# Optimization experiments

Hardware: AMD Instinct MI355X
Metric: run time of the kernel (lower is better)

The kernel has to match this reference:

```python
import math
import jax, jax.numpy as jnp
import numpy as np

DIM = 3
NB = 8  # 2**DIM blades, grade-sorted: [1, e1, e2, e3, e12, e13, e23, e123]
GRADE_SLICES = [(0, 1), (1, 4), (4, 7), (7, 8)]
SUBSPACES = [1, 3, 3, 1]
GRADE_IDX = np.repeat(np.arange(4), SUBSPACES)  # blade -> grade index
EPS = 1e-6
SQRT2 = math.sqrt(2.0)


def _build_cayley():
    # Cl(3,0) Euclidean Cayley table, blades sorted by (grade, bitmask).
    masks = sorted(range(NB), key=lambda m: (bin(m).count("1"), m))
    pos = {m: i for i, m in enumerate(masks)}
    cay = np.zeros((NB, NB, NB), dtype=np.float32)
    for i, mi in enumerate(masks):
        for k, mk in enumerate(masks):
            a, s = mi >> 1, 0
            while a:
                s += bin(a & mk).count("1")
                a >>= 1
            cay[i, pos[mi ^ mk], k] = -1.0 if (s & 1) else 1.0
    triples = []
    for gi in range(4):
        for gj in range(4):
            for gk in range(4):
                (i0, i1), (j0, j1), (k0, k1) = GRADE_SLICES[gi], GRADE_SLICES[gj], GRADE_SLICES[gk]
                if np.any(cay[i0:i1, j0:j1, k0:k1] != 0):
                    triples.append((gi, gj, gk))
    return cay, triples

CAYLEY_NP, TRIPLES = _build_cayley()
NPATHS = len(TRIPLES)  # 20 nonzero grade-triple paths for Cl(3,0)


def mv_linear(x, w, b=None):
    # x: [B,n,8]; w: [m,n,4] (one weight per grade subspace); bias -> scalar blade only.
    w8 = w[..., GRADE_IDX]  # [m,n,8]
    out = jnp.einsum("bni,mni->bmi", x, w8)
    if b is not None:
        out = out.at[..., 0].add(b)
    return out


def grade_q(x):
    # per-grade squared magnitude (Euclidean metric -> all blade signs +1): [B,n,8]->[B,n,4]
    return jnp.stack([jnp.sum(x[..., s:e] ** 2, axis=-1) for s, e in GRADE_SLICES], axis=-1)


def normalization(x, a):
    # CGENN NormalizationLayer (init=0): interpolate per-grade norm toward 1 via sigmoid gate.
    norms = jnp.sqrt(grade_q(x))  # [B,n,4]
    sa = jax.nn.sigmoid(a)  # [n,4]
    norms = sa[None] * (norms - 1.0) + 1.0
    return x / (norms[..., GRADE_IDX] + EPS)


def mv_silu(x, a, b):
    # MVSiLU with invariant='mag2': gate on [scalar, q_grade1, q_grade2, q_grade3].
    q = grade_q(x)  # [B,n,4]
    inv = jnp.concatenate([x[..., :1], q[..., 1:]], axis=-1)  # [B,n,4]
    gate = a[None] * inv + b[None]
    return jax.nn.sigmoid(gate[..., GRADE_IDX]) * x


def fc_geometric_product(x, xr, w, cayley):
    # out[b,m,j] = sum_{n,i,k} x[b,n,i] * cayley[i,j,k] * W[m,n,path(gi,gj,gk)] * xr[b,n,k]
    B, n = x.shape[0], x.shape[1]
    m = w.shape[0]
    out = jnp.zeros((B, m, NB), dtype=x.dtype)
    for t, (gi, gj, gk) in enumerate(TRIPLES):
        (i0, i1), (j0, j1), (k0, k1) = GRADE_SLICES[gi], GRADE_SLICES[gj], GRADE_SLICES[gk]
        tmp = jnp.einsum("bni,ijk,bnk->bnj", x[..., i0:i1], cayley[i0:i1, j0:j1, k0:k1], xr[..., k0:k1])
        out = out.at[:, :, j0:j1].add(jnp.einsum("bnj,mn->bmj", tmp, w[:, :, t]))
    return out


def cw_geometric_product(x, xr, w, cayley):
    # channel-wise steerable GP: out[b,n,j] = sum_{i,k} x[b,n,i]*cayley[i,j,k]*w[n,path]*xr[b,n,k]
    out = jnp.zeros_like(x)
    for t, (gi, gj, gk) in enumerate(TRIPLES):
        (i0, i1), (j0, j1), (k0, k1) = GRADE_SLICES[gi], GRADE_SLICES[gj], GRADE_SLICES[gk]
        tmp = jnp.einsum("bni,ijk,bnk->bnj", x[..., i0:i1], cayley[i0:i1, j0:j1, k0:k1], xr[..., k0:k1])
        out = out.at[:, :, j0:j1].add(tmp * w[None, :, t, None])
    return out


B, IN, HID, OUT = 1024, 256, 512, 128


def setup_inputs():
    key = jax.random.key(0)
    ks = jax.random.split(key, 16)

    def nrm(k, shape, std):
        return jax.random.normal(k, shape, dtype=jnp.float32) * std

    s_in = 1.0 / math.sqrt(IN)
    s_hid = 1.0 / math.sqrt(HID)
    return {
        "x": jax.random.normal(ks[0], (B, IN, NB), dtype=jnp.float32),
        "lr1_w": nrm(ks[1], (IN, IN, 4), s_in),
        "n1_a": jnp.zeros((IN, 4), jnp.float32),
        "ll1_w": nrm(ks[2], (HID, IN, 4), s_in),
        "ll1_b": jnp.zeros((HID,), jnp.float32),
        "w1": nrm(ks[3], (HID, IN, NPATHS), 1.0 / math.sqrt(IN * (DIM + 1))),
        "act_a": jnp.ones((HID, 4), jnp.float32),
        "act_b": jnp.zeros((HID, 4), jnp.float32),
        "lrg_w": nrm(ks[4], (HID, HID, 4), s_hid),
        "ng_a": jnp.zeros((HID, 4), jnp.float32),
        "llg_w": nrm(ks[5], (HID, HID, 4), s_hid),
        "llg_b": jnp.zeros((HID,), jnp.float32),
        "wg": nrm(ks[6], (HID, NPATHS), 1.0 / math.sqrt(DIM + 1)),
        "lr2_w": nrm(ks[7], (HID, HID, 4), s_hid),
        "n2_a": jnp.zeros((HID, 4), jnp.float32),
        "ll2_w": nrm(ks[8], (OUT, HID, 4), s_hid),
        "ll2_b": jnp.zeros((OUT,), jnp.float32),
        "w2": nrm(ks[9], (OUT, HID, NPATHS), 1.0 / math.sqrt(HID * (DIM + 1))),
    }


def reference(x, lr1_w, n1_a, ll1_w, ll1_b, w1, act_a, act_b,
              lrg_w, ng_a, llg_w, llg_b, wg,
              lr2_w, n2_a, ll2_w, ll2_b, w2):
    cayley = jnp.asarray(CAYLEY_NP)
    # fcgp1: right linear -> normalize -> weighted geometric product + first-order term
    xr = normalization(mv_linear(x, lr1_w), n1_a)
    h = (mv_linear(x, ll1_w, ll1_b) + fc_geometric_product(x, xr, w1, cayley)) / SQRT2
    h = mv_silu(h, act_a, act_b)
    # channel-wise steerable geometric product layer
    hr = normalization(mv_linear(h, lrg_w), ng_a)
    h = (mv_linear(h, llg_w, llg_b) + cw_geometric_product(h, hr, wg, cayley)) / SQRT2
    h = mv_silu(h, act_a, act_b)
    # fcgp2
    hr = normalization(mv_linear(h, lr2_w), n2_a)
    out = (mv_linear(h, ll2_w, ll2_b) + fc_geometric_product(h, hr, w2, cayley)) / SQRT2
    return out
```

## Files before the change

### kernel.cpp

```cpp
#include <hip/hip_runtime.h>
#include <math.h>


typedef unsigned short u16;
typedef __attribute__((ext_vector_type(8))) short short8;
typedef __attribute__((ext_vector_type(4))) float f32x4;

#define RSQRT2F 0.70710678118654752440f

__device__ constexpr int PP_I[64] = {
  0,0,0,0,0,0,0,0,  1,1,1,1,1,1,1,1,  2,2,2,2,2,2,2,2,  3,3,3,3,3,3,3,3,
  4,4,4,4,4,4,4,4,  5,5,5,5,5,5,5,5,  6,6,6,6,6,6,6,6,  7,7,7,7,7,7,7,7};
__device__ constexpr int PP_K[64] = {
  0,1,2,3,4,5,6,7,  0,1,2,3,4,5,6,7,  0,1,2,3,4,5,6,7,  0,1,2,3,4,5,6,7,
  0,1,2,3,4,5,6,7,  0,1,2,3,4,5,6,7,  0,1,2,3,4,5,6,7,  0,1,2,3,4,5,6,7};
__device__ constexpr int PP_C[64] = {
   0, 1, 2, 3, 4, 5, 6, 7,
   9, 8,15,16,13,14,21,20,
  10,15, 8,17,12,21,14,19,
  11,16,17, 8,21,12,13,18,
  29,24,23,35,22,34,33,28,
  30,25,35,23,34,22,32,27,
  31,35,25,24,33,32,22,26,
  43,42,41,40,39,38,37,36};
__device__ constexpr int PP_T[64] = {
   0, 1, 1, 1, 2, 2, 2, 3,
   5, 4, 7, 7, 6, 6, 9, 8,
   5, 7, 4, 7, 6, 9, 6, 8,
   5, 7, 7, 4, 9, 6, 6, 8,
  13,11,11,15,10,14,14,12,
  13,11,15,11,14,10,14,12,
  13,15,11,11,14,14,10,12,
  19,18,18,18,17,17,17,16};
__device__ constexpr int PP_J[64] = {
  0,1,2,3,4,5,6,7,
  1,0,4,5,2,3,7,6,
  2,4,0,6,1,7,3,5,
  3,5,6,0,7,1,2,4,
  4,2,1,7,0,6,5,3,
  5,3,7,1,6,0,4,2,
  6,7,3,2,5,4,0,1,
  7,6,5,4,3,2,1,0};
__device__ constexpr float PP_S[64] = {
  1, 1, 1, 1, 1, 1, 1, 1,
  1, 1, 1, 1, 1, 1, 1, 1,
  1,-1, 1, 1,-1,-1, 1,-1,
  1,-1,-1, 1, 1,-1,-1, 1,
  1,-1, 1, 1,-1,-1, 1,-1,
  1,-1,-1, 1, 1,-1,-1, 1,
  1, 1,-1, 1,-1, 1,-1,-1,
  1, 1,-1, 1,-1, 1,-1,-1};

__device__ constexpr int GJ_CNT[8] = {4,6,6,6,6,6,6,4};
__device__ constexpr int GJ_C[8][6] = {
  {0,8,22,36,0,0},
  {1,9,12,23,26,37},
  {2,10,13,24,27,38},
  {3,11,14,25,28,39},
  {4,15,18,29,32,40},
  {5,16,19,30,33,41},
  {6,17,20,31,34,42},
  {7,21,35,43,0,0}};
__device__ constexpr int GJ_T[8][6] = {
  {0,4,10,16,0,0},
  {1,5,6,11,12,17},
  {1,5,6,11,12,17},
  {1,5,6,11,12,17},
  {2,7,8,13,14,18},
  {2,7,8,13,14,18},
  {2,7,8,13,14,18},
  {3,9,15,19,0,0}};
__device__ constexpr int GRADE[8] = {0,1,1,1,2,2,2,3};

__device__ inline float sigm(float x) { return 1.0f / (1.0f + expf(-x)); }
__device__ inline u16 f2bf(float f) {
  unsigned u = __float_as_uint(f);
  return (u16)((u + 0x7fffu + ((u >> 16) & 1u)) >> 16);
}
__device__ inline float bf2f(u16 h) { return __uint_as_float(((unsigned)h) << 16); }

#define BT 128
#define MT 128
#define BKc 64

__global__ __launch_bounds__(256) void mfma_gemm(
    const u16* __restrict__ Alin, const u16* __restrict__ Pfeat,
    const u16* __restrict__ WLin, const u16* __restrict__ WLin2,
    const u16* __restrict__ WGp,
    float* __restrict__ out1, float* __restrict__ out2,
    int N, int M, int aug, int planeA, int planeO, int KSbits, int KCbits)
{
  const int zz    = blockIdx.z;
  const int set   = zz >> (3 + KSbits);
  const int rem   = zz & ((8 << KSbits) - 1);
  const int j     = rem >> KSbits;
  const int slice = rem & ((1 << KSbits) - 1);
  const u16* WL   = set ? WLin2 : WLin;
  float* outp     = set ? out2 : out1;

  const int b0   = blockIdx.y * BT;
  const int m0   = blockIdx.x * MT;
  const int tid  = threadIdx.x;
  const int lane = tid & 63;
  const int wave = tid >> 6;
  const int wr   = wave >> 1;
  const int wc   = wave & 1;
  const int l15  = lane & 15;
  const int lq   = lane >> 4;

  __shared__ u16 As[BT * BKc];
  __shared__ u16 Bs[MT * BKc];

  f32x4 zero = {0.f, 0.f, 0.f, 0.f};
  f32x4 acc[4][4];
  #pragma unroll
  for (int r = 0; r < 4; ++r)
    #pragma unroll
    for (int c = 0; c < 4; ++c) acc[r][c] = zero;

  const int g = GRADE[j];
  const int npass = aug ? (1 + GJ_CNT[j]) : 1;
  const int KC = 1 << KCbits;
  const int cper = (npass << KCbits) >> KSbits;
  const int cbeg = slice * cper;
  const int lrow = tid >> 3;
  const int lcg  = tid & 7;

  for (int ci = cbeg; ci < cbeg + cper; ++ci) {
    const int p  = ci >> KCbits;
    const int k0 = (ci & (KC - 1)) << 6;
    const u16* Abase = (p == 0) ? Alin + (size_t)j * planeA
                                : Pfeat + (size_t)GJ_C[j][p - 1] * planeA;
    const u16* Wbase = (p == 0) ? WL + (size_t)g * M * N
                                : WGp + (size_t)GJ_T[j][p - 1] * M * N;
    __syncthreads();
    #pragma unroll
    for (int q = 0; q < 4; ++q) {
      int row = lrow + q * 32;
      short8 va = *(const short8*)(Abase + (size_t)(b0 + row) * N + k0 + lcg * 8);
      *(short8*)(&As[row * BKc + (lcg ^ (row & 7)) * 8]) = va;
    }
    #pragma unroll
    for (int q = 0; q < 4; ++q) {
      int row = lrow + q * 32;
      short8 vb = *(const short8*)(Wbase + (size_t)(m0 + row) * N + k0 + lcg * 8);
      *(short8*)(&Bs[row * BKc + (lcg ^ (row & 7)) * 8]) = vb;
    }
    __syncthreads();
    #pragma unroll
    for (int s = 0; s < 2; ++s) {
      const int kq = s * 4 + lq;
      short8 af[4], bfr[4];
      #pragma unroll
      for (int r = 0; r < 4; ++r) {
        int row = wr * 64 + r * 16 + l15;
        af[r] = *(const short8*)(&As[row * BKc + (kq ^ (row & 7)) * 8]);
      }
      #pragma unroll
      for (int c = 0; c < 4; ++c) {
        int row = wc * 64 + c * 16 + l15;
        bfr[c] = *(const short8*)(&Bs[row * BKc + (kq ^ (row & 7)) * 8]);
      }
      #pragma unroll
      for (int r = 0; r < 4; ++r)
        #pragma unroll
        for (int c = 0; c < 4; ++c)
          acc[r][c] = __builtin_amdgcn_mfma_f32_16x16x32_bf16(af[r], bfr[c], acc[r][c], 0, 0, 0);
    }
  }

  float* obase = outp + (size_t)(slice * 8 + j) * planeO;
  #pragma unroll
  for (int r = 0; r < 4; ++r)
    #pragma unroll
    for (int c = 0; c < 4; ++c)
      #pragma unroll
      for (int e = 0; e < 4; ++e) {
        int bb = b0 + wr * 64 + r * 16 + lq * 4 + e;
        int mm = m0 + wc * 64 + c * 16 + l15;
        obase[(size_t)bb * M + mm] = acc[r][c][e];
      }
}

struct RepackDesc { const float* in; u16* out; int MN; int S; };
struct RepackArgs { RepackDesc d[8]; };

__global__ void repack_all(RepackArgs a)
{
  RepackDesc d = a.d[blockIdx.y];
  int mn = blockIdx.x * 256 + threadIdx.x;
  if (mn >= d.MN) return;
  if (d.S == 4) {
    float4 v = ((const float4*)d.in)[mn];
    d.out[(size_t)0 * d.MN + mn] = f2bf(v.x);
    d.out[(size_t)1 * d.MN + mn] = f2bf(v.y);
    d.out[(size_t)2 * d.MN + mn] = f2bf(v.z);
    d.out[(size_t)3 * d.MN + mn] = f2bf(v.w);
  } else {
    #pragma unroll
    for (int q = 0; q < 5; ++q) {
      float4 v = *(const float4*)(d.in + (size_t)mn * 20 + q * 4);
      d.out[(size_t)(q * 4 + 0) * d.MN + mn] = f2bf(v.x);
      d.out[(size_t)(q * 4 + 1) * d.MN + mn] = f2bf(v.y);
      d.out[(size_t)(q * 4 + 2) * d.MN + mn] = f2bf(v.z);
      d.out[(size_t)(q * 4 + 3) * d.MN + mn] = f2bf(v.w);
    }
  }
}

__global__ void xcast_kernel(const float* __restrict__ x, u16* __restrict__ xp, int PS)
{
  int t = blockIdx.x * 256 + threadIdx.x;
  if (t >= PS) return;
  float v[8];
  *(float4*)(v)     = *(const float4*)(x + (size_t)t * 8);
  *(float4*)(v + 4) = *(const float4*)(x + (size_t)t * 8 + 4);
  #pragma unroll
  for (int jj = 0; jj < 8; ++jj) xp[(size_t)jj * PS + t] = f2bf(v[jj]);
}

__global__ void pair_norm_p(const u16* __restrict__ up, const float* __restrict__ vpart,
                            const float* __restrict__ na, u16* __restrict__ Pp,
                            int PS, int M, int KS)
{
  int t = blockIdx.x * 256 + threadIdx.x;
  if (t >= PS) return;
  int m = t % M;
  float u[8], v[8];
  #pragma unroll
  for (int jj = 0; jj < 8; ++jj) {
    u[jj] = bf2f(up[(size_t)jj * PS + t]);
    float s = 0.f;
    for (int sl = 0; sl < KS; ++sl) s += vpart[(size_t)(sl * 8 + jj) * PS + t];
    v[jj] = s;
  }
  float q[4];
  q[0] = sqrtf(v[0] * v[0]);
  q[1] = sqrtf(v[1] * v[1] + v[2] * v[2] + v[3] * v[3]);
  q[2] = sqrtf(v[4] * v[4] + v[5] * v[5] + v[6] * v[6]);
  q[3] = sqrtf(v[7] * v[7]);
  float sc[4];
  #pragma unroll
  for (int gg = 0; gg < 4; ++gg) {
    float sa = sigm(na[m * 4 + gg]);
    sc[gg] = 1.0f / (sa * (q[gg] - 1.0f) + 1.0f + 1e-6f);
  }
  #pragma unroll
  for (int jj = 0; jj < 8; ++jj) v[jj] *= sc[GRADE[jj]];
  float p[44];
  #pragma unroll
  for (int c = 0; c < 44; ++c) p[c] = 0.f;
  #pragma unroll
  for (int e = 0; e < 64; ++e)
    p[PP_C[e]] += PP_S[e] * u[PP_I[e]] * v[PP_K[e]];
  #pragma unroll
  for (int c = 0; c < 44; ++c) Pp[(size_t)c * PS + t] = f2bf(p[c]);
}

__global__ void bias_silu_p(const float* __restrict__ hpart, const float* __restrict__ bias,
                            const float* __restrict__ ga, const float* __restrict__ gb,
                            u16* __restrict__ sh, int PS, int M, int KS)
{
  int t = blockIdx.x * 256 + threadIdx.x;
  if (t >= PS) return;
  int m = t % M;
  float v[8];
  #pragma unroll
  for (int jj = 0; jj < 8; ++jj) {
    float s = 0.f;
    for (int sl = 0; sl < KS; ++sl) s += hpart[(size_t)(sl * 8 + jj) * PS + t];
    v[jj] = s;
  }
  v[0] += bias[m];
  #pragma unroll
  for (int jj = 0; jj < 8; ++jj) v[jj] *= RSQRT2F;
  float inv[4];
  inv[0] = v[0];
  inv[1] = v[1]*v[1] + v[2]*v[2] + v[3]*v[3];
  inv[2] = v[4]*v[4] + v[5]*v[5] + v[6]*v[6];
  inv[3] = v[7]*v[7];
  float gt[4];
  #pragma unroll
  for (int gg = 0; gg < 4; ++gg)
    gt[gg] = sigm(ga[m * 4 + gg] * inv[gg] + gb[m * 4 + gg]);
  #pragma unroll
  for (int jj = 0; jj < 8; ++jj)
    sh[(size_t)jj * PS + t] = f2bf(v[jj] * gt[GRADE[jj]]);
}

__global__ void cw_silu_p(const float* __restrict__ llg, const u16* __restrict__ up,
                          const float* __restrict__ hrraw, const float* __restrict__ na,
                          const float* __restrict__ wg, const float* __restrict__ bias,
                          const float* __restrict__ ga, const float* __restrict__ gb,
                          u16* __restrict__ sh, int PS, int M)
{
  int t = blockIdx.x * 256 + threadIdx.x;
  if (t >= PS) return;
  int n = t % M;
  float acc[8], u[8], v[8], w[20];
  #pragma unroll
  for (int jj = 0; jj < 8; ++jj) {
    acc[jj] = llg[(size_t)jj * PS + t];
    u[jj]   = bf2f(up[(size_t)jj * PS + t]);
    v[jj]   = hrraw[(size_t)jj * PS + t];
  }
  float q[4];
  q[0] = sqrtf(v[0] * v[0]);
  q[1] = sqrtf(v[1] * v[1] + v[2] * v[2] + v[3] * v[3]);
  q[2] = sqrtf(v[4] * v[4] + v[5] * v[5] + v[6] * v[6]);
  q[3] = sqrtf(v[7] * v[7]);
  float sc[4];
  #pragma unroll
  for (int gg = 0; gg < 4; ++gg) {
    float sa = sigm(na[n * 4 + gg]);
    sc[gg] = 1.0f / (sa * (q[gg] - 1.0f) + 1.0f + 1e-6f);
  }
  #pragma unroll
  for (int jj = 0; jj < 8; ++jj) v[jj] *= sc[GRADE[jj]];
  #pragma unroll
  for (int qq = 0; qq < 5; ++qq)
    *(float4*)(w + qq * 4) = *(const float4*)(wg + (size_t)n * 20 + qq * 4);
  acc[0] += bias[n];
  #pragma unroll
  for (int e = 0; e < 64; ++e)
    acc[PP_J[e]] += PP_S[e] * u[PP_I[e]] * v[PP_K[e]] * w[PP_T[e]];
  #pragma unroll
  for (int jj = 0; jj < 8; ++jj) acc[jj] *= RSQRT2F;
  float inv[4];
  inv[0] = acc[0];
  inv[1] = acc[1]*acc[1] + acc[2]*acc[2] + acc[3]*acc[3];
  inv[2] = acc[4]*acc[4] + acc[5]*acc[5] + acc[6]*acc[6];
  inv[3] = acc[7]*acc[7];
  float gt[4];
  #pragma unroll
  for (int gg = 0; gg < 4; ++gg)
    gt[gg] = sigm(ga[n * 4 + gg] * inv[gg] + gb[n * 4 + gg]);
  #pragma unroll
  for (int jj = 0; jj < 8; ++jj)
    sh[(size_t)jj * PS + t] = f2bf(acc[jj] * gt[GRADE[jj]]);
}

__global__ void final_p(const float* __restrict__ pre, const float* __restrict__ bias,
                        float* __restrict__ outp, int PS, int M, int KS)
{
  int t = blockIdx.x * 256 + threadIdx.x;
  if (t >= PS) return;
  int m = t % M;
  float v[8];
  #pragma unroll
  for (int jj = 0; jj < 8; ++jj) {
    float s = 0.f;
    for (int sl = 0; sl < KS; ++sl) s += pre[(size_t)(sl * 8 + jj) * PS + t];
    v[jj] = s;
  }
  v[0] += bias[m];
  #pragma unroll
  for (int jj = 0; jj < 8; ++jj) v[jj] *= RSQRT2F;
  *(float4*)(outp + (size_t)t * 8)     = *(float4*)(v);
  *(float4*)(outp + (size_t)t * 8 + 4) = *(float4*)(v + 4);
}

extern "C" void kernel_launch(void* const* d_in, const int* in_sizes, int n_in,
                              void* d_out, int out_size, void* d_ws, size_t ws_size,
                              hipStream_t stream)
{
  const float* x     = (const float*)d_in[0];
  const float* lr1_w = (const float*)d_in[1];
  const float* n1_a  = (const float*)d_in[2];
  const float* ll1_w = (const float*)d_in[3];
  const float* ll1_b = (const float*)d_in[4];
  const float* w1    = (const float*)d_in[5];
  const float* act_a = (const float*)d_in[6];
  const float* act_b = (const float*)d_in[7];
  const float* lrg_w = (const float*)d_in[8];
  const float* ng_a  = (const float*)d_in[9];
  const float* llg_w = (const float*)d_in[10];
  const float* llg_b = (const float*)d_in[11];
  const float* wg    = (const float*)d_in[12];
  const float* lr2_w = (const float*)d_in[13];
  const float* n2_a  = (const float*)d_in[14];
  const float* ll2_w = (const float*)d_in[15];
  const float* ll2_b = (const float*)d_in[16];
  const float* w2    = (const float*)d_in[17];
  float* out = (float*)d_out;

  u16* W = (u16*)d_ws;
  size_t o = 0;
  u16* WL1  = W + o; o +=  262144;
  u16* WLL1 = W + o; o +=  524288;
  u16* WG1  = W + o; o += 2621440;
  u16* WLRG = W + o; o += 1048576;
  u16* WLLG = W + o; o += 1048576;
  u16* WLR2 = W + o; o += 1048576;
  u16* WLL2 = W + o; o +=  262144;
  u16* WG2  = W + o; o += 1310720;
  u16* XB   = W + o; o += 2097152;
  u16* HB   = W + o; o += 4194304;
  u16* P    = W + o; o += 23068672;
  float* f1 = (float*)(W + o);
  float* f2 = f1 + 8388608;
  float* hr   = f2;
  float* llgO = f2 + 4194304;

  dim3 blk(256);
  const int PS1 = 1024 * 256, PS2 = 1024 * 512, PSO = 1024 * 128;

  RepackArgs ra = {{
    {lr1_w, WL1, 65536, 4}, {ll1_w, WLL1, 131072, 4}, {w1, WG1, 131072, 20},
    {lrg_w, WLRG, 262144, 4}, {llg_w, WLLG, 262144, 4}, {lr2_w, WLR2, 262144, 4},
    {ll2_w, WLL2, 65536, 4}, {w2, WG2, 65536, 20}}};
  repack_all<<<dim3(1024, 8), blk, 0, stream>>>(ra);
  xcast_kernel<<<PS1 / 256, blk, 0, stream>>>(x, XB, PS1);

  mfma_gemm<<<dim3(2, 8, 16), blk, 0, stream>>>(XB, nullptr, WL1, nullptr, nullptr,
      f1, nullptr, 256, 256, 0, PS1, PS1, 1, 2);
  pair_norm_p<<<PS1 / 256, blk, 0, stream>>>(XB, f1, n1_a, P, PS1, 256, 2);
  mfma_gemm<<<dim3(4, 8, 16), blk, 0, stream>>>(XB, P, WLL1, nullptr, WG1,
      f1, nullptr, 256, 512, 1, PS1, PS2, 1, 2);
  bias_silu_p<<<PS2 / 256, blk, 0, stream>>>(f1, ll1_b, act_a, act_b, HB, PS2, 512, 2);

  mfma_gemm<<<dim3(4, 8, 16), blk, 0, stream>>>(HB, nullptr, WLRG, WLLG, nullptr,
      hr, llgO, 512, 512, 0, PS2, PS2, 0, 3);
  cw_silu_p<<<PS2 / 256, blk, 0, stream>>>(llgO, HB, hr, ng_a, wg, llg_b, act_a, act_b,
      HB, PS2, 512);

  mfma_gemm<<<dim3(4, 8, 16), blk, 0, stream>>>(HB, nullptr, WLR2, nullptr, nullptr,
      f1, nullptr, 512, 512, 0, PS2, PS2, 1, 3);
  pair_norm_p<<<PS2 / 256, blk, 0, stream>>>(HB, f1, n2_a, P, PS2, 512, 2);
  mfma_gemm<<<dim3(1, 8, 64), blk, 0, stream>>>(HB, P, WLL2, nullptr, WG2,
      f2, nullptr, 512, 128, 1, PS2, PSO, 3, 3);
  final_p<<<PSO / 256, blk, 0, stream>>>(f2, ll2_b, out, PSO, 128, 8);
}
```

Before: 266.3 us.

## Increase split-K for early GEMMs and fold x cast into repack kernel

Doubles the K-split count for the first three GEMM stages so each launches twice as many blocks. The consumer kernels now sum more fp32 partial slices, and cw_silu_p gains a split-K reduction loop. The x-to-bf16 cast moves into an extra grid row of the weight repack kernel, which saves one launch. In exchange the partial buffers double in size and the elementwise kernels read more memory, and the workspace layout changes.

```diff
diff --git a/kernel.cpp b/kernel.cpp
--- a/kernel.cpp
+++ b/kernel.cpp
@@ -183,12 +183,21 @@
 }
 
 struct RepackDesc { const float* in; u16* out; int MN; int S; };
-struct RepackArgs { RepackDesc d[8]; };
+struct RepackArgs { RepackDesc d[8]; const float* x; u16* xp; int PS; };
 
 __global__ void repack_all(RepackArgs a)
 {
+  int mn = blockIdx.x * 256 + threadIdx.x;
+  if (blockIdx.y == 8) {
+    if (mn >= a.PS) return;
+    float v[8];
+    *(float4*)(v)     = *(const float4*)(a.x + (size_t)mn * 8);
+    *(float4*)(v + 4) = *(const float4*)(a.x + (size_t)mn * 8 + 4);
+    #pragma unroll
+    for (int jj = 0; jj < 8; ++jj) a.xp[(size_t)jj * a.PS + mn] = f2bf(v[jj]);
+    return;
+  }
   RepackDesc d = a.d[blockIdx.y];
-  int mn = blockIdx.x * 256 + threadIdx.x;
   if (mn >= d.MN) return;
   if (d.S == 4) {
     float4 v = ((const float4*)d.in)[mn];
@@ -208,17 +217,6 @@
   }
 }
 
-__global__ void xcast_kernel(const float* __restrict__ x, u16* __restrict__ xp, int PS)
-{
-  int t = blockIdx.x * 256 + threadIdx.x;
-  if (t >= PS) return;
-  float v[8];
-  *(float4*)(v)     = *(const float4*)(x + (size_t)t * 8);
-  *(float4*)(v + 4) = *(const float4*)(x + (size_t)t * 8 + 4);
-  #pragma unroll
-  for (int jj = 0; jj < 8; ++jj) xp[(size_t)jj * PS + t] = f2bf(v[jj]);
-}
-
 __global__ void pair_norm_p(const u16* __restrict__ up, const float* __restrict__ vpart,
                             const float* __restrict__ na, u16* __restrict__ Pp,
                             int PS, int M, int KS)
@@ -288,11 +286,11 @@
     sh[(size_t)jj * PS + t] = f2bf(v[jj] * gt[GRADE[jj]]);
 }
 
-__global__ void cw_silu_p(const float* __restrict__ llg, const u16* __restrict__ up,
-                          const float* __restrict__ hrraw, const float* __restrict__ na,
+__global__ void cw_silu_p(const float* __restrict__ llgp, const u16* __restrict__ up,
+                          const float* __restrict__ hrp, const float* __restrict__ na,
                           const float* __restrict__ wg, const float* __restrict__ bias,
                           const float* __restrict__ ga, const float* __restrict__ gb,
-                          u16* __restrict__ sh, int PS, int M)
+                          u16* __restrict__ sh, int PS, int M, int KS)
 {
   int t = blockIdx.x * 256 + threadIdx.x;
   if (t >= PS) return;
@@ -300,9 +298,14 @@
   float acc[8], u[8], v[8], w[20];
   #pragma unroll
   for (int jj = 0; jj < 8; ++jj) {
-    acc[jj] = llg[(size_t)jj * PS + t];
+    float sl_ = 0.f, sv = 0.f;
+    for (int sl = 0; sl < KS; ++sl) {
+      sl_ += llgp[(size_t)(sl * 8 + jj) * PS + t];
+      sv  += hrp[(size_t)(sl * 8 + jj) * PS + t];
+    }
+    acc[jj] = sl_;
+    v[jj]   = sv;
     u[jj]   = bf2f(up[(size_t)jj * PS + t]);
-    v[jj]   = hrraw[(size_t)jj * PS + t];
   }
   float q[4];
   q[0] = sqrtf(v[0] * v[0]);
@@ -398,9 +401,9 @@
   u16* HB   = W + o; o += 4194304;
   u16* P    = W + o; o += 23068672;
   float* f1 = (float*)(W + o);
-  float* f2 = f1 + 8388608;
-  float* hr   = f2;
-  float* llgO = f2 + 4194304;
+  float* f2 = f1 + 16777216;
+  float* hrP  = f2;
+  float* llgP = f2 + 8388608;
 
   dim3 blk(256);
   const int PS1 = 1024 * 256, PS2 = 1024 * 512, PSO = 1024 * 128;
@@ -408,26 +411,26 @@
   RepackArgs ra = {{
     {lr1_w, WL1, 65536, 4}, {ll1_w, WLL1, 131072, 4}, {w1, WG1, 131072, 20},
     {lrg_w, WLRG, 262144, 4}, {llg_w, WLLG, 262144, 4}, {lr2_w, WLR2, 262144, 4},
-    {ll2_w, WLL2, 65536, 4}, {w2, WG2, 65536, 20}}};
-  repack_all<<<dim3(1024, 8), blk, 0, stream>>>(ra);
-  xcast_kernel<<<PS1 / 256, blk, 0, stream>>>(x, XB, PS1);
-
-  mfma_gemm<<<dim3(2, 8, 16), blk, 0, stream>>>(XB, nullptr, WL1, nullptr, nullptr,
-      f1, nullptr, 256, 256, 0, PS1, PS1, 1, 2);
-  pair_norm_p<<<PS1 / 256, blk, 0, stream>>>(XB, f1, n1_a, P, PS1, 256, 2);
-  mfma_gemm<<<dim3(4, 8, 16), blk, 0, stream>>>(XB, P, WLL1, nullptr, WG1,
-      f1, nullptr, 256, 512, 1, PS1, PS2, 1, 2);
-  bias_silu_p<<<PS2 / 256, blk, 0, stream>>>(f1, ll1_b, act_a, act_b, HB, PS2, 512, 2);
-
-  mfma_gemm<<<dim3(4, 8, 16), blk, 0, stream>>>(HB, nullptr, WLRG, WLLG, nullptr,
-      hr, llgO, 512, 512, 0, PS2, PS2, 0, 3);
-  cw_silu_p<<<PS2 / 256, blk, 0, stream>>>(llgO, HB, hr, ng_a, wg, llg_b, act_a, act_b,
-      HB, PS2, 512);
+    {ll2_w, WLL2, 65536, 4}, {w2, WG2, 65536, 20}},
+    x, XB, PS1};
+  repack_all<<<dim3(1024, 9), blk, 0, stream>>>(ra);
+
+  mfma_gemm<<<dim3(2, 8, 32), blk, 0, stream>>>(XB, nullptr, WL1, nullptr, nullptr,
+      f1, nullptr, 256, 256, 0, PS1, PS1, 2, 2);
+  pair_norm_p<<<PS1 / 256, blk, 0, stream>>>(XB, f1, n1_a, P, PS1, 256, 4);
+  mfma_gemm<<<dim3(4, 8, 32), blk, 0, stream>>>(XB, P, WLL1, nullptr, WG1,
+      f1, nullptr, 256, 512, 1, PS1, PS2, 2, 2);
+  bias_silu_p<<<PS2 / 256, blk, 0, stream>>>(f1, ll1_b, act_a, act_b, HB, PS2, 512, 4);
+
+  mfma_gemm<<<dim3(4, 8, 32), blk, 0, stream>>>(HB, nullptr, WLRG, WLLG, nullptr,
+      hrP, llgP, 512, 512, 0, PS2, PS2, 1, 3);
+  cw_silu_p<<<PS2 / 256, blk, 0, stream>>>(llgP, HB, hrP, ng_a, wg, llg_b, act_a, act_b,
+      HB, PS2, 512, 2);
 
   mfma_gemm<<<dim3(4, 8, 16), blk, 0, stream>>>(HB, nullptr, WLR2, nullptr, nullptr,
       f1, nullptr, 512, 512, 0, PS2, PS2, 1, 3);
   pair_norm_p<<<PS2 / 256, blk, 0, stream>>>(HB, f1, n2_a, P, PS2, 512, 2);
   mfma_gemm<<<dim3(1, 8, 64), blk, 0, stream>>>(HB, P, WLL2, nullptr, WG2,
-      f2, nullptr, 512, 128, 1, PS2, PSO, 3, 3);
-  final_p<<<PSO / 256, blk, 0, stream>>>(f2, ll2_b, out, PSO, 128, 8);
-}
+      f1, nullptr, 512, 128, 1, PS2, PSO, 3, 3);
+  final_p<<<PSO / 256, blk, 0, stream>>>(f1, ll2_b, out, PSO, 128, 8);
+}
```

Result: slower. 295.9 us (+11.1%).
